# Optimization experiments

Hardware: AMD Instinct MI355X
Metric: run time of the kernel (lower is better)

Reference implementation:

```python
import jax, jax.numpy as jnp
import numpy as np

G = 8      # n_group
P = 32     # input channels per group (256 // 8)
F = 64     # filters per group
KH = KW = 3
CIN = G * P   # 256
COUT = G * F  # 512


def setup_inputs() -> dict:
    key = jax.random.key(0)
    k1, k2, k3 = jax.random.split(key, 3)
    x = jax.random.normal(k1, (16, 56, 56, CIN), dtype=jnp.float32)
    kernels = jax.random.normal(k2, (G, KH, KW, P, F), dtype=jnp.float32) * 0.05
    bias = jax.random.normal(k3, (COUT,), dtype=jnp.float32) * 0.05
    return {"x": x, "kernels": kernels, "bias": bias}


def _build_dense_kernel(kernels):
    # Faithful to build_weights_for_group_conv: zero-pad each group's kernel
    # along the input-channel axis to full width, then concat along output
    # channels -> block-diagonal dense kernel [KH, KW, CIN, COUT].
    w = jnp.zeros((KH, KW, CIN, COUT), dtype=kernels.dtype)
    for i in range(G):
        w = w.at[:, :, i * P:(i + 1) * P, i * F:(i + 1) * F].set(kernels[i])
    return w


def reference(x, kernels, bias):
    w = _build_dense_kernel(kernels)
    # Single dense cuDNN-style conv over the zero-padded block-diagonal kernel,
    # exactly as tf.nn.convolution(inputs, w, strides, 'SAME', dilations).
    out = jax.lax.conv_general_dilated(
        x, w,
        window_strides=(1, 1),
        padding='SAME',
        rhs_dilation=(1, 1),
        dimension_numbers=('NHWC', 'HWIO', 'NHWC'),
    )
    return out + bias
```

## Files before the change

### kernel.cpp

```cpp
#include <hip/hip_runtime.h>

#define NG 8
#define PC 32
#define FC 64
#define HH 56
#define WW 56
#define CIN 256
#define COUT 512
#define NB 16
#define SL2 64
#define PL32 (SL2 * 128)
#define NPL 4
#define HCH 7

typedef __bf16 bf16x8 __attribute__((ext_vector_type(8)));
typedef float f32x4 __attribute__((ext_vector_type(4)));

static __device__ __forceinline__ void dma16(const void* gsrc, void* lds) {
    typedef const __attribute__((address_space(1))) unsigned int* gp_t;
    typedef __attribute__((address_space(3))) unsigned int* lp_t;
    __builtin_amdgcn_global_load_lds((gp_t)gsrc, (lp_t)lds, 16, 0, 0);
}

static __device__ __forceinline__ bf16x8 cvt8(f32x4 a, f32x4 b) {
    bf16x8 r;
    r[0] = (__bf16)a[0]; r[1] = (__bf16)a[1]; r[2] = (__bf16)a[2]; r[3] = (__bf16)a[3];
    r[4] = (__bf16)b[0]; r[5] = (__bf16)b[1]; r[6] = (__bf16)b[2]; r[7] = (__bf16)b[3];
    return r;
}

static __device__ __forceinline__ int swz32(int loc) {
    return loc ^ (((loc >> 7) & 7) << 4);
}

__global__ void cvt_w_kernel(const float* __restrict__ in,
                             __bf16* __restrict__ outb) {
    int id = blockIdx.x * blockDim.x + threadIdx.x;
    if (id >= NG * 9 * FC * PC) return;
    const int p = id & (PC - 1);
    int rest = id >> 5;
    const int f = rest & (FC - 1);
    rest >>= 6;
    const int t = rest % 9;
    const int g = rest / 9;
    outb[id] = (__bf16)in[(((size_t)(g * 9 + t)) * PC + p) * FC + f];
}

__global__ __launch_bounds__(256, 4)
void groupconv_f32dma_kernel(const float* __restrict__ x,
                             const __bf16* __restrict__ wb,
                             const float* __restrict__ bias,
                             float* __restrict__ out) {
    const int b   = blockIdx.x;
    const int g   = b & 7;
    const int hcb = (b >> 3) & 7;
    const int n   = b >> 6;
    const int h0  = hcb * HCH;

    const int tid  = threadIdx.x;
    const int wave = tid >> 6;
    const int lane = tid & 63;
    const int lo = lane & 15;
    const int hi = lane >> 4;
    const int p0 = hi * 8;
    const int fm  = (wave >> 1) * 32;
    const int wnb = (wave & 1) * 32;

    __shared__ __align__(16) unsigned char xsb[NPL * PL32];

    bf16x8 bfr[9][2];
    {
        const __bf16* wgp = wb + ((size_t)g * 9 * FC) * PC;
#pragma unroll
        for (int t = 0; t < 9; ++t)
#pragma unroll
            for (int mi = 0; mi < 2; ++mi)
                bfr[t][mi] = *reinterpret_cast<const bf16x8*>(
                    wgp + ((size_t)t * FC + (fm + mi * 16 + lo)) * PC + p0);
    }

    const int o0 = tid * 16,        o1 = (tid + 256) * 16;
    const int l0 = swz32(o0),       l1 = swz32(o1);
    const int s0 = l0 >> 7,         s1 = l1 >> 7;
    const int q0 = (l0 >> 4) & 7,   q1 = (l1 >> 4) & 7;
    const bool ok0 = (s0 >= 1 && s0 <= 56);
    const bool ok1 = (s1 >= 1 && s1 <= 56);
    const float* xg = x + ((size_t)n * HH * WW) * CIN + g * PC;
    const size_t off0 = (size_t)(s0 - 1) * CIN + q0 * 4;
    const size_t off1 = (size_t)(s1 - 1) * CIN + q1 * 4;

#pragma unroll
    for (int pl = 0; pl < NPL; ++pl) {
        unsigned char* plb = xsb + pl * PL32;
        if (!ok0 || (pl == 0 && h0 == 0))
            *reinterpret_cast<f32x4*>(plb + o0) = (f32x4)0.f;
        if (!ok1 || (pl == 0 && h0 == 0))
            *reinterpret_cast<f32x4*>(plb + o1) = (f32x4)0.f;
    }

#pragma unroll
    for (int rr = 0; rr < 3; ++rr) {
        const int r = h0 - 1 + rr;
        if (r >= 0) {
            const float* rowp = xg + (size_t)r * WW * CIN;
            void* d0 = xsb + rr * PL32 + wave * 1024;
            void* d1 = xsb + rr * PL32 + 4096 + wave * 1024;
            if (ok0) dma16(rowp + off0, d0);
            if (ok1) dma16(rowp + off1, d1);
        }
    }

    float4 bvv[2];
#pragma unroll
    for (int mi = 0; mi < 2; ++mi)
        bvv[mi] = *reinterpret_cast<const float4*>(bias + g * FC + fm + mi * 16 + hi * 4);

    float* const outg = out + ((size_t)n * HH * WW) * COUT + g * FC;

#pragma unroll
    for (int i = 0; i < HCH; ++i) {
        const int h = h0 + i;

        if (i == 0)
            asm volatile("s_waitcnt vmcnt(0) lgkmcnt(0)\n\ts_barrier" ::: "memory");
        else
            asm volatile("s_waitcnt vmcnt(4) lgkmcnt(0)\n\ts_barrier" ::: "memory");

        if (i < HCH - 1) {
            const int r = h + 2;
            unsigned char* plb = xsb + ((i + 3) % NPL) * PL32;
            if (r < HH) {
                const float* rowp = xg + (size_t)r * WW * CIN;
                if (ok0) dma16(rowp + off0, plb + (size_t)wave * 1024);
                if (ok1) dma16(rowp + off1, plb + 4096 + (size_t)wave * 1024);
            } else {
                if (ok0) *reinterpret_cast<f32x4*>(plb + o0) = (f32x4)0.f;
                if (ok1) *reinterpret_cast<f32x4*>(plb + o1) = (f32x4)0.f;
            }
        }

        f32x4 acc[2][2];
#pragma unroll
        for (int mi = 0; mi < 2; ++mi)
#pragma unroll
            for (int nj = 0; nj < 2; ++nj) acc[mi][nj] = (f32x4)0.f;

#pragma unroll
        for (int kh = 0; kh < 3; ++kh) {
            const unsigned char* plb = xsb + ((i + kh) % NPL) * PL32;
#pragma unroll
            for (int kw = 0; kw < 3; ++kw) {
                const int t = kh * 3 + kw;
                bf16x8 bx[2];
#pragma unroll
                for (int nj = 0; nj < 2; ++nj) {
                    int ss = wnb + nj * 16 + lo + kw;
                    ss = (ss > 63) ? 63 : ss;
                    const int lin = swz32(ss * 128 + hi * 32);
                    f32x4 a  = *reinterpret_cast<const f32x4*>(plb + lin);
                    f32x4 b2 = *reinterpret_cast<const f32x4*>(plb + (lin ^ 16));
                    bx[nj] = cvt8(a, b2);
                }
#pragma unroll
                for (int mi = 0; mi < 2; ++mi)
#pragma unroll
                    for (int nj = 0; nj < 2; ++nj)
                        acc[mi][nj] = __builtin_amdgcn_mfma_f32_16x16x32_bf16(
                            bfr[t][mi], bx[nj], acc[mi][nj], 0, 0, 0);
            }
        }

        float* const orow = outg + ((size_t)h * WW) * COUT;
#pragma unroll
        for (int mi = 0; mi < 2; ++mi) {
            const int f0 = fm + mi * 16 + hi * 4;
#pragma unroll
            for (int nj = 0; nj < 2; ++nj) {
                const int w = wnb + nj * 16 + lo;
                if (w < WW) {
                    f32x4 oo = acc[mi][nj];
                    oo[0] += bvv[mi].x; oo[1] += bvv[mi].y;
                    oo[2] += bvv[mi].z; oo[3] += bvv[mi].w;
                    *reinterpret_cast<f32x4*>(orow + (size_t)w * COUT + f0) = oo;
                }
            }
        }
    }
}

__global__ __launch_bounds__(256, 2)
void groupconv_f32_kernel(const float* __restrict__ x,
                          const float* __restrict__ krn,
                          const float* __restrict__ bias,
                          float* __restrict__ out) {
    const int b  = blockIdx.x;
    const int g  = b % NG;
    const int h  = (b / NG) % HH;
    const int n  = b / (NG * HH);
    const int tid = threadIdx.x;
    const int f   = tid & 63;
    const int wq  = tid >> 6;
    const int wbase = wq * 14;

    float acc[14];
#pragma unroll
    for (int i = 0; i < 14; ++i) acc[i] = 0.f;

    const float* kg = krn + (size_t)g * (9 * PC * FC);

    for (int kh = 0; kh < 3; ++kh) {
        const int hin = h + kh - 1;
        if (hin < 0 || hin >= HH) continue;
        const float* xrow = x + (((size_t)n * HH + hin) * WW) * CIN + g * PC;
        for (int pq = 0; pq < 8; ++pq) {
            float4 xv[16];
#pragma unroll
            for (int t = 0; t < 16; ++t) {
                const int win = wbase + t - 1;
                if (win >= 0 && win < WW)
                    xv[t] = *reinterpret_cast<const float4*>(xrow + (size_t)win * CIN + pq * 4);
                else
                    xv[t] = make_float4(0.f, 0.f, 0.f, 0.f);
            }
#pragma unroll
            for (int kw = 0; kw < 3; ++kw) {
                const float* kp = kg + ((kh * 3 + kw) * PC + pq * 4) * FC + f;
                const float w0 = kp[0 * FC], w1 = kp[1 * FC], w2 = kp[2 * FC], w3 = kp[3 * FC];
#pragma unroll
                for (int i = 0; i < 14; ++i) {
                    const float4 xt = xv[i + kw];
                    acc[i] = fmaf(xt.x, w0, acc[i]);
                    acc[i] = fmaf(xt.y, w1, acc[i]);
                    acc[i] = fmaf(xt.z, w2, acc[i]);
                    acc[i] = fmaf(xt.w, w3, acc[i]);
                }
            }
        }
    }

    const float bv = bias[g * FC + f];
    float* orow = out + (((size_t)n * HH + h) * WW + wbase) * COUT + g * FC + f;
#pragma unroll
    for (int i = 0; i < 14; ++i) orow[(size_t)i * COUT] = acc[i] + bv;
}

extern "C" void kernel_launch(void* const* d_in, const int* in_sizes, int n_in,
                              void* d_out, int out_size, void* d_ws, size_t ws_size,
                              hipStream_t stream) {
    const float* x    = (const float*)d_in[0];
    const float* krn  = (const float*)d_in[1];
    const float* bias = (const float*)d_in[2];
    float* out = (float*)d_out;

    const size_t w_elems = (size_t)NG * 9 * FC * PC;
    if (ws_size < w_elems * sizeof(__bf16)) {
        groupconv_f32_kernel<<<NB * HH * NG, 256, 0, stream>>>(x, krn, bias, out);
        return;
    }

    __bf16* wbuf = (__bf16*)d_ws;
    cvt_w_kernel<<<(int)((w_elems + 255) / 256), 256, 0, stream>>>(krn, wbuf);

    const int blocks = NB * 8 * NG;
    groupconv_f32dma_kernel<<<blocks, 256, 0, stream>>>(x, wbuf, bias, out);
}
```

Before: 45.40 us.

## Convert staged fp32 input rows to bf16 once per row into a rotating LDS ring

Input rows now land by DMA in two fp32 staging buffers and are converted once to bf16 into a five-plane ring, so the inner loop reads ready bf16x8 fragments directly. Before, each row was converted to bf16 three times per kw tap and again for each of three kh uses. This removes repeated LDS fp32 reads and per-use conversions from the MFMA loop. The cost is a separate conversion pass each iteration, extra barriers during setup, and a more complex double-buffered staging schedule with padded column zeroing.

```diff
diff --git a/kernel.cpp b/kernel.cpp
--- a/kernel.cpp
+++ b/kernel.cpp
@@ -8,9 +8,10 @@
 #define CIN 256
 #define COUT 512
 #define NB 16
-#define SL2 64
-#define PL32 (SL2 * 128)
-#define NPL 4
+#define SL 66
+#define PLANE (SL * 64)
+#define NPL 5
+#define PLF (64 * 128)
 #define HCH 7
 
 typedef __bf16 bf16x8 __attribute__((ext_vector_type(8)));
@@ -29,6 +30,9 @@
     return r;
 }
 
+static __device__ __forceinline__ int swz(int loc) {
+    return loc ^ (((loc >> 7) & 3) << 4);
+}
 static __device__ __forceinline__ int swz32(int loc) {
     return loc ^ (((loc >> 7) & 7) << 4);
 }
@@ -47,10 +51,10 @@
 }
 
 __global__ __launch_bounds__(256, 4)
-void groupconv_f32dma_kernel(const float* __restrict__ x,
-                             const __bf16* __restrict__ wb,
-                             const float* __restrict__ bias,
-                             float* __restrict__ out) {
+void groupconv_dcv_kernel(const float* __restrict__ x,
+                          const __bf16* __restrict__ wb,
+                          const float* __restrict__ bias,
+                          float* __restrict__ out) {
     const int b   = blockIdx.x;
     const int g   = b & 7;
     const int hcb = (b >> 3) & 7;
@@ -66,7 +70,10 @@
     const int fm  = (wave >> 1) * 32;
     const int wnb = (wave & 1) * 32;
 
-    __shared__ __align__(16) unsigned char xsb[NPL * PL32];
+    __shared__ __align__(16) unsigned char lds[2 * PLF + NPL * PLANE];
+    unsigned char* const F0 = lds;
+    unsigned char* const F1 = lds + PLF;
+    unsigned char* const Bb = lds + 2 * PLF;
 
     bf16x8 bfr[9][2];
     {
@@ -89,26 +96,55 @@
     const size_t off0 = (size_t)(s0 - 1) * CIN + q0 * 4;
     const size_t off1 = (size_t)(s1 - 1) * CIN + q1 * 4;
 
-#pragma unroll
-    for (int pl = 0; pl < NPL; ++pl) {
-        unsigned char* plb = xsb + pl * PL32;
-        if (!ok0 || (pl == 0 && h0 == 0))
-            *reinterpret_cast<f32x4*>(plb + o0) = (f32x4)0.f;
-        if (!ok1 || (pl == 0 && h0 == 0))
-            *reinterpret_cast<f32x4*>(plb + o1) = (f32x4)0.f;
-    }
-
-#pragma unroll
-    for (int rr = 0; rr < 3; ++rr) {
-        const int r = h0 - 1 + rr;
-        if (r >= 0) {
-            const float* rowp = xg + (size_t)r * WW * CIN;
-            void* d0 = xsb + rr * PL32 + wave * 1024;
-            void* d1 = xsb + rr * PL32 + 4096 + wave * 1024;
-            if (ok0) dma16(rowp + off0, d0);
-            if (ok1) dma16(rowp + off1, d1);
-        }
-    }
+    const int sc  = tid >> 2;
+    const int qc  = tid & 3;
+    const int frd = swz32(sc * 128 + qc * 32);
+    const int bwr = swz(sc * 64 + qc * 16);
+
+    if (!ok0) { *reinterpret_cast<f32x4*>(F0 + o0) = (f32x4)0.f;
+                *reinterpret_cast<f32x4*>(F1 + o0) = (f32x4)0.f; }
+    if (!ok1) { *reinterpret_cast<f32x4*>(F0 + o1) = (f32x4)0.f;
+                *reinterpret_cast<f32x4*>(F1 + o1) = (f32x4)0.f; }
+    if (tid < 180) {
+        const int q  = tid & 3;
+        const int sq = tid >> 2;
+        const int pl = sq / 9;
+        const int s  = 57 + (sq % 9);
+        *reinterpret_cast<bf16x8*>(Bb + pl * PLANE + swz(s * 64 + q * 16)) =
+            (bf16x8)(__bf16)0.f;
+    }
+
+#define STAGE(r_, Fdst)                                                         \
+    do {                                                                        \
+        const int r__ = (r_);                                                   \
+        if ((unsigned)r__ < HH) {                                               \
+            const float* rowp__ = xg + (size_t)r__ * WW * CIN;                  \
+            if (ok0) dma16(rowp__ + off0, (Fdst) + wave * 1024);                \
+            if (ok1) dma16(rowp__ + off1, (Fdst) + 4096 + wave * 1024);         \
+        } else {                                                                \
+            if (ok0) *reinterpret_cast<f32x4*>((Fdst) + o0) = (f32x4)0.f;       \
+            if (ok1) *reinterpret_cast<f32x4*>((Fdst) + o1) = (f32x4)0.f;       \
+        }                                                                       \
+    } while (0)
+
+#define CVTROW(Fsrc, Bdst)                                                      \
+    do {                                                                        \
+        f32x4 a__  = *reinterpret_cast<const f32x4*>((Fsrc) + frd);             \
+        f32x4 b2__ = *reinterpret_cast<const f32x4*>((Fsrc) + (frd ^ 16));      \
+        *reinterpret_cast<bf16x8*>((Bdst) + bwr) = cvt8(a__, b2__);             \
+    } while (0)
+
+    STAGE(h0 - 1, F0);
+    STAGE(h0,     F1);
+    asm volatile("s_waitcnt vmcnt(0) lgkmcnt(0)\n\ts_barrier" ::: "memory");
+    CVTROW(F0, Bb + 0 * PLANE);
+    CVTROW(F1, Bb + 1 * PLANE);
+    asm volatile("s_waitcnt lgkmcnt(0)\n\ts_barrier" ::: "memory");
+    STAGE(h0 + 1, F0);
+    asm volatile("s_waitcnt vmcnt(0) lgkmcnt(0)\n\ts_barrier" ::: "memory");
+    CVTROW(F0, Bb + 2 * PLANE);
+    asm volatile("s_waitcnt lgkmcnt(0)\n\ts_barrier" ::: "memory");
+    STAGE(h0 + 2, F0);
 
     float4 bvv[2];
 #pragma unroll
@@ -126,17 +162,13 @@
         else
             asm volatile("s_waitcnt vmcnt(4) lgkmcnt(0)\n\ts_barrier" ::: "memory");
 
-        if (i < HCH - 1) {
-            const int r = h + 2;
-            unsigned char* plb = xsb + ((i + 3) % NPL) * PL32;
-            if (r < HH) {
-                const float* rowp = xg + (size_t)r * WW * CIN;
-                if (ok0) dma16(rowp + off0, plb + (size_t)wave * 1024);
-                if (ok1) dma16(rowp + off1, plb + 4096 + (size_t)wave * 1024);
-            } else {
-                if (ok0) *reinterpret_cast<f32x4*>(plb + o0) = (f32x4)0.f;
-                if (ok1) *reinterpret_cast<f32x4*>(plb + o1) = (f32x4)0.f;
-            }
+        if (i <= HCH - 2) {
+            const unsigned char* Fsrc = (i & 1) ? F1 : F0;
+            CVTROW(Fsrc, Bb + ((i + 3) % NPL) * PLANE);
+        }
+        if (i <= HCH - 3) {
+            unsigned char* Fdst = ((i + 1) & 1) ? F1 : F0;
+            STAGE(h + 3, Fdst);
         }
 
         f32x4 acc[2][2];
@@ -147,19 +179,15 @@
 
 #pragma unroll
         for (int kh = 0; kh < 3; ++kh) {
-            const unsigned char* plb = xsb + ((i + kh) % NPL) * PL32;
+            const unsigned char* plb = Bb + ((i + kh) % NPL) * PLANE;
 #pragma unroll
             for (int kw = 0; kw < 3; ++kw) {
                 const int t = kh * 3 + kw;
                 bf16x8 bx[2];
 #pragma unroll
                 for (int nj = 0; nj < 2; ++nj) {
-                    int ss = wnb + nj * 16 + lo + kw;
-                    ss = (ss > 63) ? 63 : ss;
-                    const int lin = swz32(ss * 128 + hi * 32);
-                    f32x4 a  = *reinterpret_cast<const f32x4*>(plb + lin);
-                    f32x4 b2 = *reinterpret_cast<const f32x4*>(plb + (lin ^ 16));
-                    bx[nj] = cvt8(a, b2);
+                    const int ss = wnb + nj * 16 + lo + kw;
+                    bx[nj] = *reinterpret_cast<const bf16x8*>(plb + swz(ss * 64 + hi * 16));
                 }
 #pragma unroll
                 for (int mi = 0; mi < 2; ++mi)
@@ -186,6 +214,8 @@
             }
         }
     }
+#undef STAGE
+#undef CVTROW
 }
 
 __global__ __launch_bounds__(256, 2)
@@ -262,5 +292,5 @@
     cvt_w_kernel<<<(int)((w_elems + 255) / 256), 256, 0, stream>>>(krn, wbuf);
 
     const int blocks = NB * 8 * NG;
-    groupconv_f32dma_kernel<<<blocks, 256, 0, stream>>>(x, wbuf, bias, out);
-}
+    groupconv_dcv_kernel<<<blocks, 256, 0, stream>>>(x, wbuf, bias, out);
+}
```

Result: faster. 41.40 us (-8.8%).
